# Optimization experiments

Hardware: AMD Instinct MI355X
Metric: run time of the kernel (lower is better)

Reference implementation:

```python
import jax, jax.numpy as jnp
import numpy as np

N, E, G = 50000, 800000, 64
NODE_DIM, HID, HEADS, EDGE_DIM = 128, 256, 4, 2
LAYER_IN = [NODE_DIM, HID, HID]
LAYER_HEADS = [HEADS, HEADS, 1]
BN_EPS = 1e-5


def setup_inputs() -> dict:
    key = jax.random.key(0)
    ks = iter(jax.random.split(key, 80))
    def nrm(shape, s=0.05):
        return jax.random.normal(next(ks), shape, jnp.float32) * s
    inp = {}
    inp['x'] = jax.random.normal(next(ks), (N, NODE_DIM), jnp.float32)
    inp['edge_index'] = jax.random.randint(next(ks), (2, E), 0, N, jnp.int32)
    inp['edge_attr'] = jax.random.normal(next(ks), (E, EDGE_DIM), jnp.float32)
    inp['batch'] = jnp.sort(jax.random.randint(next(ks), (N,), 0, G, jnp.int32))
    for i in range(3):
        H = LAYER_HEADS[i]; C = HID // H
        inp[f'W{i}'] = nrm((LAYER_IN[i], H * C))
        inp[f'asrc{i}'] = nrm((H, C))
        inp[f'adst{i}'] = nrm((H, C))
        inp[f'We{i}'] = nrm((EDGE_DIM, H * C))
        inp[f'aedge{i}'] = nrm((H, C))
        inp[f'bconv{i}'] = jnp.zeros((HID,), jnp.float32)
        inp[f'bn{i}_g'] = jnp.ones((HID,), jnp.float32)
        inp[f'bn{i}_b'] = jnp.zeros((HID,), jnp.float32)
        inp[f'bn{i}_m'] = nrm((HID,), 0.01)
        inp[f'bn{i}_v'] = jnp.ones((HID,), jnp.float32)
    inp['Wskip'] = nrm((NODE_DIM, HID))
    inp['bskip'] = jnp.zeros((HID,), jnp.float32)
    inp['Wp1'] = nrm((2 * HID, HID))
    inp['bp1'] = jnp.zeros((HID,), jnp.float32)
    inp['Wp2'] = nrm((HID, 1))
    inp['bp2'] = jnp.zeros((1,), jnp.float32)
    return inp


def gat_conv(x, src, dst, ea, W, a_s, a_d, We, a_e, b, H, concat):
    n = x.shape[0]
    C = W.shape[1] // H
    h = (x @ W).reshape(n, H, C)                      # [N,H,C]
    # attention logits per edge (src/dst node terms + edge term)
    al = ((h * a_s).sum(-1)[src]
          + (h * a_d).sum(-1)[dst]
          + ((ea @ We).reshape(-1, H, C) * a_e).sum(-1))  # [Et,H]
    al = jax.nn.leaky_relu(al, 0.2)
    # segment softmax over destination nodes
    amax = jax.ops.segment_max(al, dst, num_segments=n)
    ex = jnp.exp(al - amax[dst])
    den = jax.ops.segment_sum(ex, dst, num_segments=n)
    alpha = ex / (den[dst] + 1e-16)
    out = jax.ops.segment_sum(h[src] * alpha[..., None], dst, num_segments=n)  # [N,H,C]
    out = out.reshape(n, H * C) if concat else out.mean(axis=1)
    return out + b


def _forward(x, edge_index, edge_attr, batch, layer_params, Wskip, bskip, Wp1, bp1, Wp2, bp2):
    n = x.shape[0]
    # add self-loops (PyG GATConv default), edge_attr filled with mean
    loop = jnp.arange(n, dtype=edge_index.dtype)
    src = jnp.concatenate([edge_index[0], loop])
    dst = jnp.concatenate([edge_index[1], loop])
    ea = jnp.concatenate([edge_attr, jnp.broadcast_to(edge_attr.mean(0), (n, edge_attr.shape[1]))], axis=0)
    identity = x
    for i, (W, a_s, a_d, We, a_e, b, g, be, rm, rv) in enumerate(layer_params):
        layer_identity = (identity @ Wskip + bskip) if i == 0 else identity
        concat = i < 2
        H = LAYER_HEADS[i]
        h = gat_conv(x, src, dst, ea, W, a_s, a_d, We, a_e, b, H, concat)
        h = (h - rm) * jax.lax.rsqrt(rv + BN_EPS) * g + be   # BatchNorm1d (eval)
        h = jax.nn.elu(h)
        x = h + layer_identity
        identity = x
    # global mean + max pool per graph
    counts = jnp.maximum(jax.ops.segment_sum(jnp.ones((n,), x.dtype), batch, num_segments=G), 1.0)
    mean_pool = jax.ops.segment_sum(x, batch, num_segments=G) / counts[:, None]
    max_pool = jax.ops.segment_max(x, batch, num_segments=G)
    emb = jnp.concatenate([mean_pool, max_pool], axis=1)      # [G, 2*HID]
    hmid = jax.nn.relu(emb @ Wp1 + bp1)
    return hmid @ Wp2 + bp2                                   # [G, 1]


def reference(x, edge_index, edge_attr, batch,
              W0, asrc0, adst0, We0, aedge0, bconv0, bn0_g, bn0_b, bn0_m, bn0_v,
              W1, asrc1, adst1, We1, aedge1, bconv1, bn1_g, bn1_b, bn1_m, bn1_v,
              W2, asrc2, adst2, We2, aedge2, bconv2, bn2_g, bn2_b, bn2_m, bn2_v,
              Wskip, bskip, Wp1, bp1, Wp2, bp2):
    layer_params = [
        (W0, asrc0, adst0, We0, aedge0, bconv0, bn0_g, bn0_b, bn0_m, bn0_v),
        (W1, asrc1, adst1, We1, aedge1, bconv1, bn1_g, bn1_b, bn1_m, bn1_v),
        (W2, asrc2, adst2, We2, aedge2, bconv2, bn2_g, bn2_b, bn2_m, bn2_v),
    ]
    return _forward(x, edge_index, edge_attr, batch, layer_params, Wskip, bskip, Wp1, bp1, Wp2, bp2)
```

## Files before the change

kernel.cpp:

```cpp
#include <hip/hip_runtime.h>
#include <cfloat>

#define Nn 50000
#define Ee 800000
#define Etot (Ee + Nn)
#define Gg 64
#define HIDc 256
#define BN_EPS 1e-5f

typedef unsigned int   uint32;
typedef unsigned short ushort16;
typedef short  bf16x8 __attribute__((ext_vector_type(8)));
typedef float  f32x4  __attribute__((ext_vector_type(4)));

__device__ inline ushort16 f2bf(float f) {
    uint32 u = __float_as_uint(f);
    u = (u + 0x7fffu + ((u >> 16) & 1u)) >> 16;
    return (ushort16)u;
}
__device__ inline float bf2f(ushort16 u) {
    return __uint_as_float(((uint32)u) << 16);
}
__device__ inline uint32 pack2(float a, float b) {
    return (uint32)f2bf(a) | ((uint32)f2bf(b) << 16);
}
__device__ inline uint32 fenc(float f) {
    uint32 b = __float_as_uint(f);
    return (b & 0x80000000u) ? ~b : (b | 0x80000000u);
}
__device__ inline float fdec(uint32 u) {
    uint32 b = (u & 0x80000000u) ? (u & 0x7fffffffu) : ~u;
    return __uint_as_float(b);
}

#define CVT4 (Nn * 128 / 4)
__global__ __launch_bounds__(256) void prep_kernel(
        const float* __restrict__ ea, float* __restrict__ ea_s,
        const float* __restrict__ We0, const float* __restrict__ ae0,
        const float* __restrict__ We1, const float* __restrict__ ae1,
        const float* __restrict__ We2, const float* __restrict__ ae2,
        float* __restrict__ M,
        const float* __restrict__ W0, const float* __restrict__ Wskip,
        const float* __restrict__ W1, const float* __restrict__ W2,
        ushort16* __restrict__ WtC, ushort16* __restrict__ Wt1,
        ushort16* __restrict__ Wt2,
        const float* __restrict__ x, ushort16* __restrict__ xbf) {
    int bid = blockIdx.x, t = threadIdx.x;
    if (bid < 256) {
        __shared__ float sh0[256], sh1[256];
        float s0 = 0.f, s1 = 0.f;
        for (int e = bid * 256 + t; e < Ee; e += 256 * 256) {
            s0 += ea[2 * e];
            s1 += ea[2 * e + 1];
        }
        sh0[t] = s0; sh1[t] = s1;
        __syncthreads();
        for (int off = 128; off > 0; off >>= 1) {
            if (t < off) { sh0[t] += sh0[t + off]; sh1[t] += sh1[t + off]; }
            __syncthreads();
        }
        if (t == 0) { atomicAdd(&ea_s[0], sh0[0]); atomicAdd(&ea_s[1], sh1[0]); }
    } else if (bid == 256) {
        if (t >= 18) return;
        int l = t < 8 ? 0 : (t < 16 ? 1 : 2);
        int r = t - l * 8;
        const float* We = (l == 0) ? We0 : (l == 1 ? We1 : We2);
        const float* ae = (l == 0) ? ae0 : (l == 1 ? ae1 : ae2);
        int Hl = (l < 2) ? 4 : 1;
        int Cl = 256 / Hl;
        int d = r / Hl, hh = r % Hl;
        float s = 0.f;
        for (int c = 0; c < Cl; ++c)
            s += We[d * 256 + hh * Cl + c] * ae[hh * Cl + c];
        M[l * 8 + r] = s;
    } else if (bid < 385) {
        int k = bid - 257;
        WtC[(long)t * 128 + k] = f2bf(W0[(long)k * 256 + t]);
    } else if (bid < 513) {
        int k = bid - 385;
        WtC[(long)(256 + t) * 128 + k] = f2bf(Wskip[(long)k * 256 + t]);
    } else if (bid < 769) {
        int k = bid - 513;
        Wt1[(long)t * 256 + k] = f2bf(W1[(long)k * 256 + t]);
    } else if (bid < 1025) {
        int k = bid - 769;
        Wt2[(long)t * 256 + k] = f2bf(W2[(long)k * 256 + t]);
    } else {
        int i = (bid - 1025) * 256 + t;
        if (i < CVT4) {
            float4 v = *(const float4*)&x[i * 4];
            ushort4 o;
            o.x = f2bf(v.x); o.y = f2bf(v.y); o.z = f2bf(v.z); o.w = f2bf(v.w);
            *(ushort4*)&xbf[i * 4] = o;
        }
    }
}

__global__ void hist_kernel(const int* __restrict__ ei, int* __restrict__ counts) {
    int e = blockIdx.x * blockDim.x + threadIdx.x;
    if (e >= Etot) return;
    int d = (e < Ee) ? ei[Ee + e] : (e - Ee);
    atomicAdd(&counts[d], 1);
}

__global__ void scan1_kernel(const int* __restrict__ in, int* __restrict__ inc,
                             int* __restrict__ bsums) {
    __shared__ int sh[256];
    int i = blockIdx.x * 256 + threadIdx.x;
    int v = (i < Nn) ? in[i] : 0;
    sh[threadIdx.x] = v;
    __syncthreads();
    for (int off = 1; off < 256; off <<= 1) {
        int t = ((int)threadIdx.x >= off) ? sh[threadIdx.x - off] : 0;
        __syncthreads();
        sh[threadIdx.x] += t;
        __syncthreads();
    }
    if (i < Nn) inc[i] = sh[threadIdx.x];
    if (threadIdx.x == 255) bsums[blockIdx.x] = sh[255];
}

__global__ void scan23_kernel(const int* __restrict__ inc, const int* __restrict__ bsums,
                              int* __restrict__ row_start, int* __restrict__ cursor, int nb) {
    __shared__ int sh[256];
    int b = blockIdx.x, t = threadIdx.x;
    sh[t] = (t < b && t < nb) ? bsums[t] : 0;
    __syncthreads();
    for (int off = 128; off > 0; off >>= 1) {
        if (t < off) sh[t] += sh[t + off];
        __syncthreads();
    }
    int base = sh[0];
    int i = b * 256 + t;
    if (i < Nn) {
        int v = inc[i] + base;
        row_start[i + 1] = v;
        cursor[i + 1] = v;
    }
    if (i == 0) { row_start[0] = 0; cursor[0] = 0; }
}

__global__ void scatter_kernel(const int* __restrict__ ei, const float* __restrict__ ea,
                               const float* __restrict__ ea_sum, int* __restrict__ cursor,
                               int* __restrict__ src_sorted, float* __restrict__ ea_sorted) {
    int e = blockIdx.x * blockDim.x + threadIdx.x;
    if (e >= Etot) return;
    int s, d; float e0, e1;
    if (e < Ee) {
        s = ei[e]; d = ei[Ee + e];
        e0 = ea[2 * e]; e1 = ea[2 * e + 1];
    } else {
        s = d = e - Ee;
        const float invE = 1.f / (float)Ee;
        e0 = ea_sum[0] * invE; e1 = ea_sum[1] * invE;
    }
    int pos = atomicAdd(&cursor[d], 1);
    src_sorted[pos] = s;
    ea_sorted[2 * pos]     = e0;
    ea_sorted[2 * pos + 1] = e1;
}

#define LDK 40
__global__ __launch_bounds__(256) void mfma_gemm_kernel(
        const ushort16* __restrict__ A,
        const ushort16* __restrict__ Wt,
        uint32* __restrict__ outF,
        uint32* __restrict__ outS,
        const float* __restrict__ bskip,
        const float* __restrict__ a_s, const float* __restrict__ a_d,
        float* __restrict__ ssrc, float* __restrict__ sdst,
        int n, int K) {
    __shared__ ushort16 As[128 * LDK];
    __shared__ ushort16 Bs[128 * LDK];
    const int t    = threadIdx.x;
    const int row0 = blockIdx.x * 128;
    const int c0   = blockIdx.y * 128;
    const bool isSkip = (outS != nullptr) && (c0 >= 256);
    const int cc0  = isSkip ? c0 - 256 : c0;
    const int wave = t >> 6, lane = t & 63;
    const int wr = wave >> 1, wc = wave & 1;
    const int l15 = lane & 15, quad = lane >> 4;

    f32x4 acc[4][4];
#pragma unroll
    for (int j = 0; j < 4; ++j)
#pragma unroll
        for (int i = 0; i < 4; ++i) {
            acc[j][i][0] = 0.f; acc[j][i][1] = 0.f;
            acc[j][i][2] = 0.f; acc[j][i][3] = 0.f;
        }

    const int sm = t & 127;
    const int so = t >> 7;

    for (int k0 = 0; k0 < K; k0 += 32) {
#pragma unroll
        for (int h = 0; h < 2; ++h) {
            int oct = so + 2 * h;
            int grow = row0 + sm;
            uint4 va = make_uint4(0, 0, 0, 0);
            if (grow < n) va = *(const uint4*)&A[(long)grow * K + k0 + 8 * oct];
            *(uint4*)&As[sm * LDK + 8 * oct] = va;
            *(uint4*)&Bs[sm * LDK + 8 * oct] =
                *(const uint4*)&Wt[(long)(c0 + sm) * K + k0 + 8 * oct];
        }
        __syncthreads();
        bf16x8 af[4], bfv[4];
#pragma unroll
        for (int i = 0; i < 4; ++i) {
            af[i]  = *(const bf16x8*)&As[(wr * 64 + i * 16 + l15) * LDK + quad * 8];
            bfv[i] = *(const bf16x8*)&Bs[(wc * 64 + i * 16 + l15) * LDK + quad * 8];
        }
#pragma unroll
        for (int j = 0; j < 4; ++j)
#pragma unroll
            for (int i = 0; i < 4; ++i)
                acc[j][i] = __builtin_amdgcn_mfma_f32_16x16x32_bf16(
                    bfv[j], af[i], acc[j][i], 0, 0, 0);
        __syncthreads();
    }

    float4 bb[4];
#pragma unroll
    for (int j = 0; j < 4; ++j) {
        if (isSkip) bb[j] = *(const float4*)&bskip[cc0 + wc * 64 + j * 16 + quad * 4];
        else        bb[j] = make_float4(0.f, 0.f, 0.f, 0.f);
    }

    uint32* tgt = isSkip ? outS : outF;
#pragma unroll
    for (int i = 0; i < 4; ++i) {
        int row = row0 + wr * 64 + i * 16 + l15;
        if (row >= n) continue;
#pragma unroll
        for (int j = 0; j < 4; ++j) {
            int col = cc0 + wc * 64 + j * 16 + quad * 4;
            uint2 pk;
            pk.x = pack2(acc[j][i][0] + bb[j].x, acc[j][i][1] + bb[j].y);
            pk.y = pack2(acc[j][i][2] + bb[j].z, acc[j][i][3] + bb[j].w);
            *(uint2*)&tgt[(long)row * 128 + (col >> 1)] = pk;
        }
    }

    if (!isSkip && a_s != nullptr) {
        float4 asv[4], adv[4];
#pragma unroll
        for (int j = 0; j < 4; ++j) {
            int col = cc0 + wc * 64 + j * 16 + quad * 4;
            asv[j] = *(const float4*)&a_s[col];
            adv[j] = *(const float4*)&a_d[col];
        }
        const int part = (cc0 + wc * 64) >> 6;
#pragma unroll
        for (int i = 0; i < 4; ++i) {
            float ps = 0.f, pd = 0.f;
#pragma unroll
            for (int j = 0; j < 4; ++j) {
                ps += acc[j][i][0] * asv[j].x + acc[j][i][1] * asv[j].y
                    + acc[j][i][2] * asv[j].z + acc[j][i][3] * asv[j].w;
                pd += acc[j][i][0] * adv[j].x + acc[j][i][1] * adv[j].y
                    + acc[j][i][2] * adv[j].z + acc[j][i][3] * adv[j].w;
            }
            ps += __shfl_xor(ps, 16); ps += __shfl_xor(ps, 32);
            pd += __shfl_xor(pd, 16); pd += __shfl_xor(pd, 32);
            if (quad == 0) {
                int row = row0 + wr * 64 + i * 16 + l15;
                if (row < n) {
                    ssrc[row * 4 + part] = ps;
                    sdst[row * 4 + part] = pd;
                }
            }
        }
    }
}

template <int H>
__global__ __launch_bounds__(256) void edge_softmax_kernel(
        const int* __restrict__ src_sorted, const int* __restrict__ row_start,
        const float* __restrict__ ea_sorted, const float* __restrict__ ssrc,
        const float* __restrict__ sdst, const float* __restrict__ M,
        float* __restrict__ w) {
    int node = (blockIdx.x * blockDim.x + threadIdx.x) >> 6;
    int lane = threadIdx.x & 63;
    if (node >= Nn) return;
    int beg = row_start[node], end = row_start[node + 1];
    int deg = end - beg;
    float sd[H], M0[H], M1[H], m[H], den[H];
    if (H == 4) {
#pragma unroll
        for (int h = 0; h < H; ++h) sd[h] = sdst[node * 4 + h];
    } else {
        float4 v = *(const float4*)&sdst[node * 4];
        sd[0] = v.x + v.y + v.z + v.w;
    }
#pragma unroll
    for (int h = 0; h < H; ++h) {
        M0[h] = M[h]; M1[h] = M[H + h];
        m[h] = -FLT_MAX; den[h] = 0.f;
    }
    auto ssval = [&](int s, int h) -> float {
        if (H == 4) return ssrc[s * 4 + h];
        float4 v = *(const float4*)&ssrc[s * 4];
        return v.x + v.y + v.z + v.w;
    };
    if (deg <= 256) {
        float lreg[4][H];
#pragma unroll
        for (int k = 0; k < 4; ++k) {
            int idx = beg + lane + (k << 6);
            if (idx < end) {
                int s = src_sorted[idx];
                float e0 = ea_sorted[2 * idx], e1 = ea_sorted[2 * idx + 1];
#pragma unroll
                for (int h = 0; h < H; ++h) {
                    float l = ssval(s, h) + sd[h] + e0 * M0[h] + e1 * M1[h];
                    l = (l > 0.f) ? l : 0.2f * l;
                    lreg[k][h] = l;
                    if (l > m[h]) { den[h] = den[h] * __expf(m[h] - l) + 1.f; m[h] = l; }
                    else den[h] += __expf(l - m[h]);
                }
            }
        }
#pragma unroll
        for (int h = 0; h < H; ++h) {
            for (int off = 32; off > 0; off >>= 1) {
                float om = __shfl_down(m[h], off);
                float od = __shfl_down(den[h], off);
                float nm = fmaxf(m[h], om);
                den[h] = den[h] * __expf(m[h] - nm) + od * __expf(om - nm);
                m[h] = nm;
            }
            m[h]   = __shfl(m[h], 0);
            den[h] = __shfl(den[h], 0);
            den[h] = 1.f / (den[h] + 1e-16f);
        }
#pragma unroll
        for (int k = 0; k < 4; ++k) {
            int idx = beg + lane + (k << 6);
            if (idx < end) {
#pragma unroll
                for (int h = 0; h < H; ++h)
                    w[(long)idx * H + h] = __expf(lreg[k][h] - m[h]) * den[h];
            }
        }
    } else {
        for (int idx = beg + lane; idx < end; idx += 64) {
            int s = src_sorted[idx];
            float e0 = ea_sorted[2 * idx], e1 = ea_sorted[2 * idx + 1];
#pragma unroll
            for (int h = 0; h < H; ++h) {
                float l = ssval(s, h) + sd[h] + e0 * M0[h] + e1 * M1[h];
                l = (l > 0.f) ? l : 0.2f * l;
                w[(long)idx * H + h] = l;
                if (l > m[h]) { den[h] = den[h] * __expf(m[h] - l) + 1.f; m[h] = l; }
                else den[h] += __expf(l - m[h]);
            }
        }
#pragma unroll
        for (int h = 0; h < H; ++h) {
            for (int off = 32; off > 0; off >>= 1) {
                float om = __shfl_down(m[h], off);
                float od = __shfl_down(den[h], off);
                float nm = fmaxf(m[h], om);
                den[h] = den[h] * __expf(m[h] - nm) + od * __expf(om - nm);
                m[h] = nm;
            }
            m[h]   = __shfl(m[h], 0);
            den[h] = __shfl(den[h], 0);
            den[h] = 1.f / (den[h] + 1e-16f);
        }
        for (int idx = beg + lane; idx < end; idx += 64) {
#pragma unroll
            for (int h = 0; h < H; ++h) {
                float l = w[(long)idx * H + h];
                w[(long)idx * H + h] = __expf(l - m[h]) * den[h];
            }
        }
    }
}

__global__ __launch_bounds__(128) void agg_kernel(
        const int* __restrict__ src_sorted, const int* __restrict__ row_start,
        const uint32* __restrict__ hbuf2, const float* __restrict__ w,
        const float* __restrict__ bconv,
        const float* __restrict__ bn_g, const float* __restrict__ bn_b,
        const float* __restrict__ bn_m, const float* __restrict__ bn_v,
        const uint32* __restrict__ identity2, uint32* __restrict__ out2, int H) {
    int node = blockIdx.x;
    int c2 = threadIdx.x;
    int C2 = 128 / H;
    int hh = c2 / C2;
    int beg = row_start[node], end = row_start[node + 1];
    float a0 = 0.f, a1 = 0.f;
    for (int idx = beg; idx < end; idx += 4) {
        int   s[4];
        float ww[4];
#pragma unroll
        for (int k = 0; k < 4; ++k) {
            int j = idx + k;
            bool ok = j < end;
            int jj = ok ? j : beg;
            s[k]  = src_sorted[jj];
            ww[k] = ok ? w[(long)jj * H + hh] : 0.f;
        }
#pragma unroll
        for (int k = 0; k < 4; ++k) {
            uint32 u = hbuf2[(long)s[k] * 128 + c2];
            float lo = __uint_as_float(u << 16);
            float hi = __uint_as_float(u & 0xffff0000u);
            a0 += ww[k] * lo;
            a1 += ww[k] * hi;
        }
    }
    int c = 2 * c2;
    float v0 = a0 + bconv[c];
    float v1 = a1 + bconv[c + 1];
    v0 = (v0 - bn_m[c])     * rsqrtf(bn_v[c]     + BN_EPS) * bn_g[c]     + bn_b[c];
    v1 = (v1 - bn_m[c + 1]) * rsqrtf(bn_v[c + 1] + BN_EPS) * bn_g[c + 1] + bn_b[c + 1];
    v0 = (v0 > 0.f) ? v0 : (expf(v0) - 1.f);
    v1 = (v1 > 0.f) ? v1 : (expf(v1) - 1.f);
    uint32 idu = identity2[(long)node * 128 + c2];
    v0 += __uint_as_float(idu << 16);
    v1 += __uint_as_float(idu & 0xffff0000u);
    out2[(long)node * 128 + c2] = (uint32)f2bf(v0) | ((uint32)f2bf(v1) << 16);
}

#define POOL_ROWS 32
__global__ __launch_bounds__(128) void pool_kernel(
        const uint32* __restrict__ x2, const int* __restrict__ batch,
        float* __restrict__ psum, uint32* __restrict__ pmax, float* __restrict__ pcnt) {
    int c2 = threadIdx.x;
    int n0 = blockIdx.x * POOL_ROWS;
    if (n0 >= Nn) return;
    int n1 = min(n0 + POOL_ROWS, Nn);
    int cur = batch[n0];
    float s0 = 0.f, s1 = 0.f, m0 = -FLT_MAX, m1 = -FLT_MAX;
    int cnt = 0;
    int c = 2 * c2;
    for (int i = n0; i < n1; ++i) {
        int g = batch[i];
        if (g != cur) {
            atomicAdd(&psum[cur * 256 + c], s0);
            atomicAdd(&psum[cur * 256 + c + 1], s1);
            atomicMax(&pmax[cur * 256 + c], fenc(m0));
            atomicMax(&pmax[cur * 256 + c + 1], fenc(m1));
            if (c2 == 0) atomicAdd(&pcnt[cur], (float)cnt);
            cur = g; s0 = s1 = 0.f; m0 = m1 = -FLT_MAX; cnt = 0;
        }
        uint32 u = x2[(long)i * 128 + c2];
        float lo = __uint_as_float(u << 16);
        float hi = __uint_as_float(u & 0xffff0000u);
        s0 += lo; s1 += hi;
        m0 = fmaxf(m0, lo); m1 = fmaxf(m1, hi);
        ++cnt;
    }
    atomicAdd(&psum[cur * 256 + c], s0);
    atomicAdd(&psum[cur * 256 + c + 1], s1);
    atomicMax(&pmax[cur * 256 + c], fenc(m0));
    atomicMax(&pmax[cur * 256 + c + 1], fenc(m1));
    if (c2 == 0) atomicAdd(&pcnt[cur], (float)cnt);
}

__global__ __launch_bounds__(256) void mlp_kernel(
        const float* __restrict__ psum, const uint32* __restrict__ pmax,
        const float* __restrict__ pcnt, const float* __restrict__ Wp1,
        const float* __restrict__ bp1, const float* __restrict__ Wp2,
        const float* __restrict__ bp2, float* __restrict__ out) {
    int g = blockIdx.x;
    int j = threadIdx.x;
    float inv = 1.f / fmaxf(pcnt[g], 1.f);
    float acc = bp1[j];
    for (int k = 0; k < 256; ++k)
        acc += (psum[g * 256 + k] * inv) * Wp1[k * 256 + j];
    for (int k = 0; k < 256; ++k)
        acc += fdec(pmax[g * 256 + k]) * Wp1[(256 + k) * 256 + j];
    float v = fmaxf(acc, 0.f) * Wp2[j];
    __shared__ float red[256];
    red[j] = v;
    __syncthreads();
    for (int off = 128; off > 0; off >>= 1) {
        if (j < off) red[j] += red[j + off];
        __syncthreads();
    }
    if (j == 0) out[g] = red[0] + bp2[0];
}

extern "C" void kernel_launch(void* const* d_in, const int* in_sizes, int n_in,
                              void* d_out, int out_size, void* d_ws, size_t ws_size,
                              hipStream_t stream) {
    const float* x   = (const float*)d_in[0];
    const int*   ei  = (const int*)d_in[1];
    const float* ea  = (const float*)d_in[2];
    const int*   bat = (const int*)d_in[3];
    auto LP = [&](int l, int j) { return (const float*)d_in[4 + l * 10 + j]; };
    const float* Wskip = (const float*)d_in[34];
    const float* bskip = (const float*)d_in[35];
    const float* Wp1   = (const float*)d_in[36];
    const float* bp1   = (const float*)d_in[37];
    const float* Wp2   = (const float*)d_in[38];
    const float* bp2   = (const float*)d_in[39];
    float* out = (float*)d_out;

    char* p = (char*)d_ws;
    auto alloc = [&](size_t bytes) { void* r = (void*)p; p += (bytes + 255) & ~(size_t)255; return r; };
    uint32*   hbuf2  = (uint32*)alloc((size_t)Nn * 256 * 2);
    uint32*   skipbf = (uint32*)alloc((size_t)Nn * 128 * 4);
    uint32*   resA   = (uint32*)alloc((size_t)Nn * 128 * 4);
    uint32*   resB   = (uint32*)alloc((size_t)Nn * 128 * 4);
    ushort16* xbf    = (ushort16*)alloc((size_t)Nn * 128 * 2);
    float*    wbuf   = (float*)alloc((size_t)Etot * 4 * 4);
    float*    ea_sorted = (float*)alloc((size_t)Etot * 2 * 4);
    float*    ssrc   = (float*)alloc((size_t)Nn * 4 * 4);
    float*    sdst   = (float*)alloc((size_t)Nn * 4 * 4);
    int*      counts = (int*)alloc((size_t)Nn * 4);
    int*      incb   = (int*)alloc((size_t)Nn * 4);
    int*      row_start = (int*)alloc((size_t)(Nn + 1) * 4);
    int*      cursor    = (int*)alloc((size_t)(Nn + 1) * 4);
    int*      src_sorted = (int*)alloc((size_t)Etot * 4);
    int*      bsums  = (int*)alloc(256 * 4);
    float*    ea_s   = (float*)alloc(2 * 4);
    float*    Mbuf   = (float*)alloc(32 * 4);
    ushort16* WtC    = (ushort16*)alloc((size_t)512 * 128 * 2);
    ushort16* Wt1    = (ushort16*)alloc((size_t)256 * 256 * 2);
    ushort16* Wt2    = (ushort16*)alloc((size_t)256 * 256 * 2);
    float*    psum   = (float*)alloc((size_t)Gg * 256 * 4);
    uint32*   pmax   = (uint32*)alloc((size_t)Gg * 256 * 4);
    float*    pcnt   = (float*)alloc((size_t)Gg * 4);

    const int nb = (Nn + 255) / 256;
    const int ebks = (Etot + 255) / 256;
    const int wgrid = (Nn * 64 + 255) / 256;

    hipMemsetAsync(counts, 0, (size_t)Nn * 4, stream);
    hipMemsetAsync(ea_s, 0, 8, stream);
    hipMemsetAsync(psum, 0, (size_t)Gg * 256 * 4 * 2 + (size_t)Gg * 4, stream);

    prep_kernel<<<1025 + (CVT4 + 255) / 256, 256, 0, stream>>>(
        ea, ea_s, LP(0,3), LP(0,4), LP(1,3), LP(1,4), LP(2,3), LP(2,4), Mbuf,
        LP(0,0), Wskip, LP(1,0), LP(2,0), WtC, Wt1, Wt2, x, xbf);

    hist_kernel<<<ebks, 256, 0, stream>>>(ei, counts);
    scan1_kernel<<<nb, 256, 0, stream>>>(counts, incb, bsums);
    scan23_kernel<<<nb, 256, 0, stream>>>(incb, bsums, row_start, cursor, nb);
    scatter_kernel<<<ebks, 256, 0, stream>>>(ei, ea, ea_s, cursor, src_sorted, ea_sorted);

    {
        dim3 g0((Nn + 127) / 128, 4);
        mfma_gemm_kernel<<<g0, 256, 0, stream>>>(
            xbf, WtC, hbuf2, skipbf, bskip,
            LP(0,1), LP(0,2), ssrc, sdst, Nn, 128);
    }

    const uint32* lid[3] = { skipbf, resA, resB };
    uint32*       lou[3] = { resA, resB, resA };
    const int     Hh[3]  = { 4, 4, 1 };
    const ushort16* lain[3] = { nullptr, (ushort16*)resA, (ushort16*)resB };
    const ushort16* lwt[3]  = { nullptr, Wt1, Wt2 };
    for (int l = 0; l < 3; ++l) {
        const int H = Hh[l];
        if (l > 0) {
            dim3 gl((Nn + 127) / 128, 2);
            mfma_gemm_kernel<<<gl, 256, 0, stream>>>(
                lain[l], lwt[l], hbuf2, nullptr, nullptr,
                LP(l,1), LP(l,2), ssrc, sdst, Nn, 256);
        }
        if (H == 4)
            edge_softmax_kernel<4><<<wgrid, 256, 0, stream>>>(
                src_sorted, row_start, ea_sorted, ssrc, sdst, Mbuf + l * 8, wbuf);
        else
            edge_softmax_kernel<1><<<wgrid, 256, 0, stream>>>(
                src_sorted, row_start, ea_sorted, ssrc, sdst, Mbuf + l * 8, wbuf);
        agg_kernel<<<Nn, 128, 0, stream>>>(src_sorted, row_start, hbuf2, wbuf,
            LP(l,5), LP(l,6), LP(l,7), LP(l,8), LP(l,9), lid[l], lou[l], H);
    }

    pool_kernel<<<(Nn + POOL_ROWS - 1) / POOL_ROWS, 128, 0, stream>>>(resA, bat, psum, pmax, pcnt);
    mlp_kernel<<<Gg, 256, 0, stream>>>(psum, pmax, pcnt, Wp1, bp1, Wp2, bp2, out);
}
```

Baseline: 726.3 us.

## Fuse edge softmax into aggregation, pre-swizzle GEMM weights, merge histogram into prep

The edge-softmax pass is folded into the per-node aggregation kernel. One wave computes the normalized attention weights into shared memory, and the block then aggregates, so the per-edge weight buffer round trip through global memory is skipped for nodes of degree up to 256. GEMM weights are pre-laid out in MFMA fragment order, so each lane loads its B operand directly from global memory, removing the B shared-memory tile. The destination histogram is merged into the prep kernel launch to cut a kernel launch. The tradeoff is that only one of two waves works during the softmax phase, and the B loads now come from global memory every k-step.

```diff
diff --git a/kernel.cpp b/kernel.cpp
--- a/kernel.cpp
+++ b/kernel.cpp
@@ -18,9 +18,6 @@
     u = (u + 0x7fffu + ((u >> 16) & 1u)) >> 16;
     return (ushort16)u;
 }
-__device__ inline float bf2f(ushort16 u) {
-    return __uint_as_float(((uint32)u) << 16);
-}
 __device__ inline uint32 pack2(float a, float b) {
     return (uint32)f2bf(a) | ((uint32)f2bf(b) << 16);
 }
@@ -33,7 +30,14 @@
     return __uint_as_float(b);
 }
 
+__device__ inline long ws_index(int c, int k, int KB) {
+    int cb = c >> 4, m = c & 15, kb = k >> 5, q = (k >> 3) & 3, e = k & 7;
+    return (((long)(cb * KB + kb) * 64 + q * 16 + m) << 3) + e;
+}
+
 #define CVT4 (Nn * 128 / 4)
+#define CVT_BLKS ((CVT4 + 255) / 256)
+#define EBKS ((Etot + 255) / 256)
 __global__ __launch_bounds__(256) void prep_kernel(
         const float* __restrict__ ea, float* __restrict__ ea_s,
         const float* __restrict__ We0, const float* __restrict__ ae0,
@@ -44,7 +48,8 @@
         const float* __restrict__ W1, const float* __restrict__ W2,
         ushort16* __restrict__ WtC, ushort16* __restrict__ Wt1,
         ushort16* __restrict__ Wt2,
-        const float* __restrict__ x, ushort16* __restrict__ xbf) {
+        const float* __restrict__ x, ushort16* __restrict__ xbf,
+        const int* __restrict__ ei, int* __restrict__ counts) {
     int bid = blockIdx.x, t = threadIdx.x;
     if (bid < 256) {
         __shared__ float sh0[256], sh1[256];
@@ -75,17 +80,17 @@
         M[l * 8 + r] = s;
     } else if (bid < 385) {
         int k = bid - 257;
-        WtC[(long)t * 128 + k] = f2bf(W0[(long)k * 256 + t]);
+        WtC[ws_index(t, k, 4)] = f2bf(W0[(long)k * 256 + t]);
     } else if (bid < 513) {
         int k = bid - 385;
-        WtC[(long)(256 + t) * 128 + k] = f2bf(Wskip[(long)k * 256 + t]);
+        WtC[ws_index(256 + t, k, 4)] = f2bf(Wskip[(long)k * 256 + t]);
     } else if (bid < 769) {
         int k = bid - 513;
-        Wt1[(long)t * 256 + k] = f2bf(W1[(long)k * 256 + t]);
+        Wt1[ws_index(t, k, 8)] = f2bf(W1[(long)k * 256 + t]);
     } else if (bid < 1025) {
         int k = bid - 769;
-        Wt2[(long)t * 256 + k] = f2bf(W2[(long)k * 256 + t]);
-    } else {
+        Wt2[ws_index(t, k, 8)] = f2bf(W2[(long)k * 256 + t]);
+    } else if (bid < 1025 + CVT_BLKS) {
         int i = (bid - 1025) * 256 + t;
         if (i < CVT4) {
             float4 v = *(const float4*)&x[i * 4];
@@ -93,14 +98,13 @@
             o.x = f2bf(v.x); o.y = f2bf(v.y); o.z = f2bf(v.z); o.w = f2bf(v.w);
             *(ushort4*)&xbf[i * 4] = o;
         }
-    }
-}
-
-__global__ void hist_kernel(const int* __restrict__ ei, int* __restrict__ counts) {
-    int e = blockIdx.x * blockDim.x + threadIdx.x;
-    if (e >= Etot) return;
-    int d = (e < Ee) ? ei[Ee + e] : (e - Ee);
-    atomicAdd(&counts[d], 1);
+    } else {
+        int e = (bid - 1025 - CVT_BLKS) * 256 + t;
+        if (e < Etot) {
+            int d = (e < Ee) ? ei[Ee + e] : (e - Ee);
+            atomicAdd(&counts[d], 1);
+        }
+    }
 }
 
 __global__ void scan1_kernel(const int* __restrict__ in, int* __restrict__ inc,
@@ -163,7 +167,7 @@
 #define LDK 40
 __global__ __launch_bounds__(256) void mfma_gemm_kernel(
         const ushort16* __restrict__ A,
-        const ushort16* __restrict__ Wt,
+        const ushort16* __restrict__ WS,
         uint32* __restrict__ outF,
         uint32* __restrict__ outS,
         const float* __restrict__ bskip,
@@ -171,7 +175,6 @@
         float* __restrict__ ssrc, float* __restrict__ sdst,
         int n, int K) {
     __shared__ ushort16 As[128 * LDK];
-    __shared__ ushort16 Bs[128 * LDK];
     const int t    = threadIdx.x;
     const int row0 = blockIdx.x * 128;
     const int c0   = blockIdx.y * 128;
@@ -180,6 +183,7 @@
     const int wave = t >> 6, lane = t & 63;
     const int wr = wave >> 1, wc = wave & 1;
     const int l15 = lane & 15, quad = lane >> 4;
+    const int KB = K >> 5;
 
     f32x4 acc[4][4];
 #pragma unroll
@@ -194,6 +198,7 @@
     const int so = t >> 7;
 
     for (int k0 = 0; k0 < K; k0 += 32) {
+        const int kb = k0 >> 5;
 #pragma unroll
         for (int h = 0; h < 2; ++h) {
             int oct = so + 2 * h;
@@ -201,16 +206,18 @@
             uint4 va = make_uint4(0, 0, 0, 0);
             if (grow < n) va = *(const uint4*)&A[(long)grow * K + k0 + 8 * oct];
             *(uint4*)&As[sm * LDK + 8 * oct] = va;
-            *(uint4*)&Bs[sm * LDK + 8 * oct] =
-                *(const uint4*)&Wt[(long)(c0 + sm) * K + k0 + 8 * oct];
-        }
-        __syncthreads();
-        bf16x8 af[4], bfv[4];
-#pragma unroll
-        for (int i = 0; i < 4; ++i) {
-            af[i]  = *(const bf16x8*)&As[(wr * 64 + i * 16 + l15) * LDK + quad * 8];
-            bfv[i] = *(const bf16x8*)&Bs[(wc * 64 + i * 16 + l15) * LDK + quad * 8];
-        }
+        }
+        bf16x8 bfv[4];
+#pragma unroll
+        for (int j = 0; j < 4; ++j) {
+            int cb = ((c0 + wc * 64) >> 4) + j;
+            bfv[j] = *(const bf16x8*)&WS[(((long)cb * KB + kb) * 64 + lane) << 3];
+        }
+        __syncthreads();
+        bf16x8 af[4];
+#pragma unroll
+        for (int i = 0; i < 4; ++i)
+            af[i] = *(const bf16x8*)&As[(wr * 64 + i * 16 + l15) * LDK + quad * 8];
 #pragma unroll
         for (int j = 0; j < 4; ++j)
 #pragma unroll
@@ -275,122 +282,122 @@
 }
 
 template <int H>
-__global__ __launch_bounds__(256) void edge_softmax_kernel(
+__global__ __launch_bounds__(128) void agg_kernel(
         const int* __restrict__ src_sorted, const int* __restrict__ row_start,
         const float* __restrict__ ea_sorted, const float* __restrict__ ssrc,
         const float* __restrict__ sdst, const float* __restrict__ M,
-        float* __restrict__ w) {
-    int node = (blockIdx.x * blockDim.x + threadIdx.x) >> 6;
-    int lane = threadIdx.x & 63;
-    if (node >= Nn) return;
+        float* __restrict__ wbig,
+        const uint32* __restrict__ hbuf2, const float* __restrict__ bconv,
+        const float* __restrict__ bn_g, const float* __restrict__ bn_b,
+        const float* __restrict__ bn_m, const float* __restrict__ bn_v,
+        const uint32* __restrict__ identity2, uint32* __restrict__ out2) {
+    __shared__ float shw[256 * H];
+    int node = blockIdx.x;
+    int t = threadIdx.x;
     int beg = row_start[node], end = row_start[node + 1];
     int deg = end - beg;
-    float sd[H], M0[H], M1[H], m[H], den[H];
-    if (H == 4) {
-#pragma unroll
-        for (int h = 0; h < H; ++h) sd[h] = sdst[node * 4 + h];
-    } else {
-        float4 v = *(const float4*)&sdst[node * 4];
-        sd[0] = v.x + v.y + v.z + v.w;
-    }
-#pragma unroll
-    for (int h = 0; h < H; ++h) {
-        M0[h] = M[h]; M1[h] = M[H + h];
-        m[h] = -FLT_MAX; den[h] = 0.f;
-    }
-    auto ssval = [&](int s, int h) -> float {
-        if (H == 4) return ssrc[s * 4 + h];
-        float4 v = *(const float4*)&ssrc[s * 4];
-        return v.x + v.y + v.z + v.w;
-    };
-    if (deg <= 256) {
-        float lreg[4][H];
-#pragma unroll
-        for (int k = 0; k < 4; ++k) {
-            int idx = beg + lane + (k << 6);
-            if (idx < end) {
+    bool big = deg > 256;
+
+    if (t < 64) {
+        int lane = t;
+        float sd[H], M0[H], M1[H], m[H], den[H];
+        if (H == 4) {
+#pragma unroll
+            for (int h = 0; h < H; ++h) sd[h] = sdst[node * 4 + h];
+        } else {
+            float4 v = *(const float4*)&sdst[node * 4];
+            sd[0] = v.x + v.y + v.z + v.w;
+        }
+#pragma unroll
+        for (int h = 0; h < H; ++h) {
+            M0[h] = M[h]; M1[h] = M[H + h];
+            m[h] = -FLT_MAX; den[h] = 0.f;
+        }
+        auto ssval = [&](int s, int h) -> float {
+            if (H == 4) return ssrc[s * 4 + h];
+            float4 v = *(const float4*)&ssrc[s * 4];
+            return v.x + v.y + v.z + v.w;
+        };
+        if (!big) {
+            float lreg[4][H];
+#pragma unroll
+            for (int k = 0; k < 4; ++k) {
+                int idx = beg + lane + (k << 6);
+                if (idx < end) {
+                    int s = src_sorted[idx];
+                    float e0 = ea_sorted[2 * idx], e1 = ea_sorted[2 * idx + 1];
+#pragma unroll
+                    for (int h = 0; h < H; ++h) {
+                        float l = ssval(s, h) + sd[h] + e0 * M0[h] + e1 * M1[h];
+                        l = (l > 0.f) ? l : 0.2f * l;
+                        lreg[k][h] = l;
+                        if (l > m[h]) { den[h] = den[h] * __expf(m[h] - l) + 1.f; m[h] = l; }
+                        else den[h] += __expf(l - m[h]);
+                    }
+                }
+            }
+#pragma unroll
+            for (int h = 0; h < H; ++h) {
+                for (int off = 32; off > 0; off >>= 1) {
+                    float om = __shfl_down(m[h], off);
+                    float od = __shfl_down(den[h], off);
+                    float nm = fmaxf(m[h], om);
+                    den[h] = den[h] * __expf(m[h] - nm) + od * __expf(om - nm);
+                    m[h] = nm;
+                }
+                m[h]   = __shfl(m[h], 0);
+                den[h] = __shfl(den[h], 0);
+                den[h] = 1.f / (den[h] + 1e-16f);
+            }
+#pragma unroll
+            for (int k = 0; k < 4; ++k) {
+                int idx = beg + lane + (k << 6);
+                if (idx < end) {
+#pragma unroll
+                    for (int h = 0; h < H; ++h)
+                        shw[(idx - beg) * H + h] = __expf(lreg[k][h] - m[h]) * den[h];
+                }
+            }
+        } else {
+            for (int idx = beg + lane; idx < end; idx += 64) {
                 int s = src_sorted[idx];
                 float e0 = ea_sorted[2 * idx], e1 = ea_sorted[2 * idx + 1];
 #pragma unroll
                 for (int h = 0; h < H; ++h) {
                     float l = ssval(s, h) + sd[h] + e0 * M0[h] + e1 * M1[h];
                     l = (l > 0.f) ? l : 0.2f * l;
-                    lreg[k][h] = l;
+                    wbig[(long)idx * H + h] = l;
                     if (l > m[h]) { den[h] = den[h] * __expf(m[h] - l) + 1.f; m[h] = l; }
                     else den[h] += __expf(l - m[h]);
                 }
             }
-        }
-#pragma unroll
-        for (int h = 0; h < H; ++h) {
-            for (int off = 32; off > 0; off >>= 1) {
-                float om = __shfl_down(m[h], off);
-                float od = __shfl_down(den[h], off);
-                float nm = fmaxf(m[h], om);
-                den[h] = den[h] * __expf(m[h] - nm) + od * __expf(om - nm);
-                m[h] = nm;
-            }
-            m[h]   = __shfl(m[h], 0);
-            den[h] = __shfl(den[h], 0);
-            den[h] = 1.f / (den[h] + 1e-16f);
-        }
-#pragma unroll
-        for (int k = 0; k < 4; ++k) {
-            int idx = beg + lane + (k << 6);
-            if (idx < end) {
-#pragma unroll
-                for (int h = 0; h < H; ++h)
-                    w[(long)idx * H + h] = __expf(lreg[k][h] - m[h]) * den[h];
-            }
-        }
-    } else {
-        for (int idx = beg + lane; idx < end; idx += 64) {
-            int s = src_sorted[idx];
-            float e0 = ea_sorted[2 * idx], e1 = ea_sorted[2 * idx + 1];
 #pragma unroll
             for (int h = 0; h < H; ++h) {
-                float l = ssval(s, h) + sd[h] + e0 * M0[h] + e1 * M1[h];
-                l = (l > 0.f) ? l : 0.2f * l;
-                w[(long)idx * H + h] = l;
-                if (l > m[h]) { den[h] = den[h] * __expf(m[h] - l) + 1.f; m[h] = l; }
-                else den[h] += __expf(l - m[h]);
-            }
-        }
-#pragma unroll
-        for (int h = 0; h < H; ++h) {
-            for (int off = 32; off > 0; off >>= 1) {
-                float om = __shfl_down(m[h], off);
-                float od = __shfl_down(den[h], off);
-                float nm = fmaxf(m[h], om);
-                den[h] = den[h] * __expf(m[h] - nm) + od * __expf(om - nm);
-                m[h] = nm;
-            }
-            m[h]   = __shfl(m[h], 0);
-            den[h] = __shfl(den[h], 0);
-            den[h] = 1.f / (den[h] + 1e-16f);
-        }
-        for (int idx = beg + lane; idx < end; idx += 64) {
-#pragma unroll
-            for (int h = 0; h < H; ++h) {
-                float l = w[(long)idx * H + h];
-                w[(long)idx * H + h] = __expf(l - m[h]) * den[h];
-            }
-        }
-    }
-}
-
-__global__ __launch_bounds__(128) void agg_kernel(
-        const int* __restrict__ src_sorted, const int* __restrict__ row_start,
-        const uint32* __restrict__ hbuf2, const float* __restrict__ w,
-        const float* __restrict__ bconv,
-        const float* __restrict__ bn_g, const float* __restrict__ bn_b,
-        const float* __restrict__ bn_m, const float* __restrict__ bn_v,
-        const uint32* __restrict__ identity2, uint32* __restrict__ out2, int H) {
-    int node = blockIdx.x;
-    int c2 = threadIdx.x;
-    int C2 = 128 / H;
+                for (int off = 32; off > 0; off >>= 1) {
+                    float om = __shfl_down(m[h], off);
+                    float od = __shfl_down(den[h], off);
+                    float nm = fmaxf(m[h], om);
+                    den[h] = den[h] * __expf(m[h] - nm) + od * __expf(om - nm);
+                    m[h] = nm;
+                }
+                m[h]   = __shfl(m[h], 0);
+                den[h] = __shfl(den[h], 0);
+                den[h] = 1.f / (den[h] + 1e-16f);
+            }
+            for (int idx = beg + lane; idx < end; idx += 64) {
+#pragma unroll
+                for (int h = 0; h < H; ++h) {
+                    float l = wbig[(long)idx * H + h];
+                    wbig[(long)idx * H + h] = __expf(l - m[h]) * den[h];
+                }
+            }
+        }
+    }
+    __syncthreads();
+
+    int c2 = t;
+    const int C2 = 128 / H;
     int hh = c2 / C2;
-    int beg = row_start[node], end = row_start[node + 1];
     float a0 = 0.f, a1 = 0.f;
     for (int idx = beg; idx < end; idx += 4) {
         int   s[4];
@@ -401,7 +408,8 @@
             bool ok = j < end;
             int jj = ok ? j : beg;
             s[k]  = src_sorted[jj];
-            ww[k] = ok ? w[(long)jj * H + hh] : 0.f;
+            float wv = big ? wbig[(long)jj * H + hh] : shw[(jj - beg) * H + hh];
+            ww[k] = ok ? wv : 0.f;
         }
 #pragma unroll
         for (int k = 0; k < 4; ++k) {
@@ -422,7 +430,7 @@
     uint32 idu = identity2[(long)node * 128 + c2];
     v0 += __uint_as_float(idu << 16);
     v1 += __uint_as_float(idu & 0xffff0000u);
-    out2[(long)node * 128 + c2] = (uint32)f2bf(v0) | ((uint32)f2bf(v1) << 16);
+    out2[(long)node * 128 + c2] = pack2(v0, v1);
 }
 
 #define POOL_ROWS 32
@@ -528,21 +536,18 @@
     float*    pcnt   = (float*)alloc((size_t)Gg * 4);
 
     const int nb = (Nn + 255) / 256;
-    const int ebks = (Etot + 255) / 256;
-    const int wgrid = (Nn * 64 + 255) / 256;
 
     hipMemsetAsync(counts, 0, (size_t)Nn * 4, stream);
     hipMemsetAsync(ea_s, 0, 8, stream);
     hipMemsetAsync(psum, 0, (size_t)Gg * 256 * 4 * 2 + (size_t)Gg * 4, stream);
 
-    prep_kernel<<<1025 + (CVT4 + 255) / 256, 256, 0, stream>>>(
+    prep_kernel<<<1025 + CVT_BLKS + EBKS, 256, 0, stream>>>(
         ea, ea_s, LP(0,3), LP(0,4), LP(1,3), LP(1,4), LP(2,3), LP(2,4), Mbuf,
-        LP(0,0), Wskip, LP(1,0), LP(2,0), WtC, Wt1, Wt2, x, xbf);
-
-    hist_kernel<<<ebks, 256, 0, stream>>>(ei, counts);
+        LP(0,0), Wskip, LP(1,0), LP(2,0), WtC, Wt1, Wt2, x, xbf, ei, counts);
+
     scan1_kernel<<<nb, 256, 0, stream>>>(counts, incb, bsums);
     scan23_kernel<<<nb, 256, 0, stream>>>(incb, bsums, row_start, cursor, nb);
-    scatter_kernel<<<ebks, 256, 0, stream>>>(ei, ea, ea_s, cursor, src_sorted, ea_sorted);
+    scatter_kernel<<<EBKS, 256, 0, stream>>>(ei, ea, ea_s, cursor, src_sorted, ea_sorted);
 
     {
         dim3 g0((Nn + 127) / 128, 4);
@@ -565,13 +570,13 @@
                 LP(l,1), LP(l,2), ssrc, sdst, Nn, 256);
         }
         if (H == 4)
-            edge_softmax_kernel<4><<<wgrid, 256, 0, stream>>>(
-                src_sorted, row_start, ea_sorted, ssrc, sdst, Mbuf + l * 8, wbuf);
+            agg_kernel<4><<<Nn, 128, 0, stream>>>(
+                src_sorted, row_start, ea_sorted, ssrc, sdst, Mbuf + l * 8, wbuf,
+                hbuf2, LP(l,5), LP(l,6), LP(l,7), LP(l,8), LP(l,9), lid[l], lou[l]);
         else
-            edge_softmax_kernel<1><<<wgrid, 256, 0, stream>>>(
-                src_sorted, row_start, ea_sorted, ssrc, sdst, Mbuf + l * 8, wbuf);
-        agg_kernel<<<Nn, 128, 0, stream>>>(src_sorted, row_start, hbuf2, wbuf,
-            LP(l,5), LP(l,6), LP(l,7), LP(l,8), LP(l,9), lid[l], lou[l], H);
+            agg_kernel<1><<<Nn, 128, 0, stream>>>(
+                src_sorted, row_start, ea_sorted, ssrc, sdst, Mbuf + l * 8, wbuf,
+                hbuf2, LP(l,5), LP(l,6), LP(l,7), LP(l,8), LP(l,9), lid[l], lou[l]);
     }
 
     pool_kernel<<<(Nn + POOL_ROWS - 1) / POOL_ROWS, 128, 0, stream>>>(resA, bat, psum, pmax, pcnt);
```

Result: faster. 709.0 us (-2.4%).
